# Performance work log

Hardware: AMD Instinct MI355X
Metric: run time of the kernel (lower is better)

Reference implementation:

```python
import jax, jax.numpy as jnp
import numpy as np

N_NODES = 20000
N_INPUT = 64
K_MAX = 12
BITS = 64
N_OUT = 10
BATCH = 64
T = 128


def setup_inputs() -> dict:
    key = jax.random.key(0)
    ks = jax.random.split(key, 8)
    x = jax.random.randint(ks[0], (BATCH, T, BITS), 0, 2, dtype=jnp.int32)
    w_in = jax.random.randint(ks[1], (BITS, N_INPUT), 0, 2, dtype=jnp.int32)
    adj_list = jax.random.randint(ks[2], (N_NODES, K_MAX), 0, N_NODES, dtype=jnp.int32)
    adj_mask = jax.random.randint(ks[3], (N_NODES, K_MAX), 0, 2, dtype=jnp.int32)
    lut = jax.random.randint(ks[4], (N_NODES, 2 ** K_MAX), 0, 2, dtype=jnp.int32)
    init_states = jax.random.randint(ks[5], (1, N_NODES), 0, 2, dtype=jnp.int32)
    W_out = jax.random.normal(ks[6], (N_OUT, N_NODES - N_INPUT), dtype=jnp.float32) * 0.02
    b_out = jnp.zeros((N_OUT,), dtype=jnp.float32)
    return {"x": x, "w_in": w_in, "adj_list": adj_list, "adj_mask": adj_mask,
            "lut": lut, "init_states": init_states, "W_out": W_out, "b_out": b_out}


def reference(x, w_in, adj_list, adj_mask, lut, init_states, W_out, b_out):
    B, T_, bits = x.shape
    N, k = adj_list.shape
    I = w_in.shape[1]
    # powers_of_2, big-endian order as in make_minimal_powers_of_two (flip)
    powers = (2 ** jnp.arange(k - 1, -1, -1)).astype(jnp.int32)  # [k]
    no_neigh = ~(adj_mask.astype(bool).any(axis=1))              # [N] nodes w/o neighbours keep state
    node_ids = jnp.arange(N)
    states0 = jnp.broadcast_to(init_states, (B, N)).astype(jnp.int32)

    def step(states, x_t):
        # inject input: bipartite mapping of input bits onto first I nodes (OR-combine)
        u = ((x_t @ w_in) > 0).astype(jnp.int32)                 # [B, I]
        states = states.at[:, :I].set(u)
        # gather incoming neighbour states per node (irregular gather)
        neigh = jnp.take(states, adj_list, axis=1)               # [B, N, k]
        neigh = neigh * adj_mask[None, :, :]
        # bit-pack into LUT index
        idx = (neigh * powers[None, None, :]).sum(axis=-1)       # [B, N], < 2^k
        new = lut[node_ids[None, :], idx]                        # [B, N] LUT lookup
        new = jnp.where(no_neigh[None, :], states, new)
        return new, None

    states, _ = jax.lax.scan(step, states0, jnp.swapaxes(x, 0, 1))
    # readout on reservoir (non-input) nodes at final timestep
    feats = states[:, I:].astype(jnp.float32)                    # [B, N-I]
    out = jax.nn.sigmoid(feats @ W_out.T + b_out)                # [B, n_outputs]
    return out
```

## Files before the change

### kernel.cpp

```cpp
#include <hip/hip_runtime.h>
#include <cstdint>
#include <cstddef>


#define N_NODES   20000
#define N_INPUT   64
#define K_MAX     12
#define T_STEPS   128
#define N_BATCH   64
#define N_OUT     10
#define N_FEAT    (N_NODES - N_INPUT)
#define DUMMY_NODE 20000
#define ST_WORDS  20004

#define NBLK 512
#define NTHR 512
#define NPB  39
#define NPB_PAD 40
#define BAR_CNT 64
#define GO_CNT  8
#define BAR_STRIDE 32

typedef unsigned long long u64;

__global__ __launch_bounds__(256) void pack_x_kernel(const int* __restrict__ x,
                                                     u64* __restrict__ xp) {
  const int t = blockIdx.x;
  const int wave = threadIdx.x >> 6, lane = threadIdx.x & 63;
  for (int b = wave; b < N_BATCH; b += 4) {
    int v = x[((size_t)b * T_STEPS + t) * 64 + lane];
    u64 bal = __ballot(v != 0);
    if (lane == 0) xp[(size_t)t * N_BATCH + b] = bal;
  }
}

__global__ __launch_bounds__(256) void init_kernel(const int* __restrict__ inis,
                                                   const int* __restrict__ w_in,
                                                   const u64* __restrict__ xp,
                                                   u64* __restrict__ buf0,
                                                   u64* __restrict__ buf1,
                                                   u64* __restrict__ wcol,
                                                   unsigned* __restrict__ bar) {
  if (blockIdx.x < 79) {
    int n = blockIdx.x * 256 + threadIdx.x;
    if (n >= N_INPUT && n < ST_WORDS) {
      u64 w = (n < N_NODES && inis[n] != 0) ? ~0ull : 0ull;
      buf0[n] = w;
      buf1[n] = w;
    }
  } else {
    const int wave = threadIdx.x >> 6, lane = threadIdx.x & 63;
    u64 xw = xp[lane];
    for (int i = wave; i < 64; i += 4) {
      int wv = w_in[(size_t)lane * 64 + i];
      u64 wc = __ballot(wv != 0);
      if (lane == 0) wcol[i] = wc;
      u64 ub = __ballot((xw & wc) != 0);
      if (lane == 0) buf0[i] = ub;
    }
    if (threadIdx.x < BAR_CNT + GO_CNT)
      bar[threadIdx.x * BAR_STRIDE] = 0u;
  }
}

__global__ __launch_bounds__(64) void u_pre_kernel(const u64* __restrict__ xp,
                                                   const u64* __restrict__ wcol,
                                                   u64* __restrict__ u_all) {
  const int t = blockIdx.x, lane = threadIdx.x;
  u64 xw = xp[(size_t)t * N_BATCH + lane];
  for (int i = 0; i < 64; i++) {
    u64 ub = __ballot((xw & wcol[i]) != 0);
    if (lane == 0) u_all[(size_t)t * 64 + i] = ub;
  }
}

__device__ __forceinline__ u64 bit_transpose64(u64 w, int lane) {
  const u64 LO0 = 0x00000000FFFFFFFFull, LO1 = 0x0000FFFF0000FFFFull,
            LO2 = 0x00FF00FF00FF00FFull, LO3 = 0x0F0F0F0F0F0F0F0Full,
            LO4 = 0x3333333333333333ull, LO5 = 0x5555555555555555ull;
#define XP_STAGE(d, LO)                                                  \
  {                                                                      \
    u64 p = (u64)__shfl_xor((long long)w, (d), 64);                      \
    if (lane & (d)) w = ((p >> (d)) & (LO)) | (w & ~(LO));               \
    else            w = (w & (LO)) | ((p << (d)) & ~(LO));               \
  }
  XP_STAGE(32, LO0) XP_STAGE(16, LO1) XP_STAGE(8, LO2)
  XP_STAGE(4,  LO3) XP_STAGE(2,  LO4) XP_STAGE(1, LO5)
#undef XP_STAGE
  return w;
}

__global__ __launch_bounds__(NTHR, 4) void reservoir_kernel(
    const int* __restrict__ lut, const int* __restrict__ adj,
    const int* __restrict__ mask, const u64* __restrict__ u_all,
    u64* __restrict__ buf0, u64* __restrict__ buf1,
    unsigned* __restrict__ bar) {
  __shared__ u64 lut_lds[NPB_PAD * 64];
  __shared__ int adj_lds[NPB_PAD * K_MAX];
  __shared__ unsigned char hn_lds[NPB_PAD];

  const int bi = blockIdx.x;
  const int tid = threadIdx.x;
  const int wave = tid >> 6, lane = tid & 63;
  const int base = N_INPUT + bi * NPB;
  const int nloc = min(NPB, N_NODES - base);

  if (tid < NPB_PAD) {
    int i = tid, h = 0;
    if (i < nloc) {
      for (int j = 0; j < K_MAX; j++) {
        int m = mask[(size_t)(base + i) * K_MAX + j];
        int a = adj[(size_t)(base + i) * K_MAX + j];
        adj_lds[i * K_MAX + (K_MAX - 1 - j)] = m ? a : DUMMY_NODE;
        h |= m;
      }
    } else {
      for (int j = 0; j < K_MAX; j++) adj_lds[i * K_MAX + j] = DUMMY_NODE;
    }
    hn_lds[i] = (unsigned char)(h ? 1 : 0);
  }

  const int nwords = nloc * 64;
  const int* lp = lut + (size_t)base * 4096;
  for (int w0 = wave * 8; w0 < nwords; w0 += 64) {
    int v[8];
#pragma unroll
    for (int q = 0; q < 8; q++) {
      int widx = w0 + q;
      v[q] = (widx < nwords) ? lp[(size_t)widx * 64 + lane] : 0;
    }
#pragma unroll
    for (int q = 0; q < 8; q++) {
      int widx = w0 + q;
      u64 bal = __ballot(v[q] != 0);
      if (lane == 0 && widx < nwords) lut_lds[widx] = bal;
    }
  }
  __syncthreads();

  const int l0 = wave * 5;
  const int cnt = min(5, nloc - l0);

  int my_a = DUMMY_NODE;
  if (lane < 60) my_a = adj_lds[l0 * K_MAX + lane];
  unsigned hmask = 0;
#pragma unroll
  for (int i = 0; i < 5; i++) hmask |= (unsigned)hn_lds[l0 + i] << i;

  for (int t = 0; t < T_STEPS; t++) {
    u64* cur = (t & 1) ? buf1 : buf0;
    u64* nxt = (t & 1) ? buf0 : buf1;

    u64 w = __hip_atomic_load(&cur[my_a], __ATOMIC_RELAXED,
                              __HIP_MEMORY_SCOPE_AGENT);
    w = bit_transpose64(w, lane);

#pragma unroll
    for (int i = 0; i < 5; i++) {
      if (i < cnt) {
        unsigned idx = (unsigned)(w >> (12 * i)) & 0xFFFu;
        u64 g = lut_lds[(l0 + i) * 64 + (idx >> 6)];
        u64 res = __ballot((g >> (idx & 63)) & 1ull);
        if (lane == 0 && ((hmask >> i) & 1u))
          __hip_atomic_store(&nxt[base + l0 + i], res,
                             __ATOMIC_RELAXED, __HIP_MEMORY_SCOPE_AGENT);
      }
    }

    if (bi == NBLK - 1 && wave == 7 && t + 1 < T_STEPS) {
      u64 uw = u_all[(size_t)(t + 1) * 64 + lane];
      __hip_atomic_store(&nxt[lane], uw, __ATOMIC_RELAXED, __HIP_MEMORY_SCOPE_AGENT);
    }

    if (t != T_STEPS - 1) {
      __syncthreads();
      __builtin_amdgcn_fence(__ATOMIC_RELEASE, "workgroup");
      if (tid == 0)
        __hip_atomic_fetch_add(&bar[(bi & (BAR_CNT - 1)) * BAR_STRIDE], 1u,
                               __ATOMIC_RELAXED, __HIP_MEMORY_SCOPE_AGENT);
      if (bi == 0 && wave == 0) {
        const unsigned tgt = (unsigned)(t + 1) * (NBLK / BAR_CNT);
        for (;;) {
          unsigned c = __hip_atomic_load(&bar[lane * BAR_STRIDE],
                                         __ATOMIC_RELAXED, __HIP_MEMORY_SCOPE_AGENT);
          if (__all(c >= tgt)) break;
        }
        if (lane < GO_CNT)
          __hip_atomic_store(&bar[(BAR_CNT + lane) * BAR_STRIDE], (unsigned)(t + 1),
                             __ATOMIC_RELAXED, __HIP_MEMORY_SCOPE_AGENT);
      } else if (wave == 0) {
        unsigned* gp = &bar[(BAR_CNT + (bi & (GO_CNT - 1))) * BAR_STRIDE];
        while (__hip_atomic_load(gp, __ATOMIC_RELAXED, __HIP_MEMORY_SCOPE_AGENT)
               < (unsigned)(t + 1)) {  }
      }
      __builtin_amdgcn_fence(__ATOMIC_ACQUIRE, "workgroup");
      __syncthreads();
    }
  }
}

__global__ __launch_bounds__(256) void readout_kernel(const u64* __restrict__ st,
                                                      const float* __restrict__ Wout,
                                                      const float* __restrict__ bout,
                                                      float* __restrict__ out) {
  const int b = blockIdx.x / N_OUT;
  const int o = blockIdx.x % N_OUT;
  float acc = 0.f;
  for (int n = threadIdx.x; n < N_FEAT; n += 256) {
    u64 s = st[N_INPUT + n];
    float w = Wout[(size_t)o * N_FEAT + n];
    acc += ((s >> b) & 1ull) ? w : 0.f;
  }
  for (int off = 32; off > 0; off >>= 1) acc += __shfl_down(acc, off);
  __shared__ float red[4];
  const int wave = threadIdx.x >> 6, lane = threadIdx.x & 63;
  if (lane == 0) red[wave] = acc;
  __syncthreads();
  if (threadIdx.x == 0) {
    float tot = red[0] + red[1] + red[2] + red[3] + bout[o];
    out[(size_t)b * N_OUT + o] = 1.f / (1.f + __expf(-tot));
  }
}

extern "C" void kernel_launch(void* const* d_in, const int* in_sizes, int n_in,
                              void* d_out, int out_size, void* d_ws, size_t ws_size,
                              hipStream_t stream) {
  const int* x    = (const int*)d_in[0];
  const int* w_in = (const int*)d_in[1];
  const int* adj  = (const int*)d_in[2];
  const int* mask = (const int*)d_in[3];
  const int* lut  = (const int*)d_in[4];
  const int* inis = (const int*)d_in[5];
  const float* Wout = (const float*)d_in[6];
  const float* bout = (const float*)d_in[7];
  float* out = (float*)d_out;

  char* ws = (char*)d_ws;
  size_t off = 0;
  auto alloc = [&](size_t bytes) -> void* {
    void* p = ws + off;
    off += (bytes + 255) & ~(size_t)255;
    return p;
  };
  u64* buf0 = (u64*)alloc((size_t)ST_WORDS * 8);
  u64* buf1 = (u64*)alloc((size_t)ST_WORDS * 8);
  u64* xp   = (u64*)alloc((size_t)T_STEPS * N_BATCH * 8);
  u64* wcol = (u64*)alloc(64 * 8);
  u64* u_all = (u64*)alloc((size_t)T_STEPS * 64 * 8);
  unsigned* bar = (unsigned*)alloc((size_t)(BAR_CNT + GO_CNT) * BAR_STRIDE * 4);
  (void)ws_size; (void)in_sizes; (void)n_in; (void)out_size;

  hipLaunchKernelGGL(pack_x_kernel, dim3(T_STEPS), dim3(256), 0, stream, x, xp);
  hipLaunchKernelGGL(init_kernel, dim3(80), dim3(256), 0, stream,
                     inis, w_in, xp, buf0, buf1, wcol, bar);
  hipLaunchKernelGGL(u_pre_kernel, dim3(T_STEPS), dim3(64), 0, stream,
                     xp, wcol, u_all);

  hipLaunchKernelGGL(reservoir_kernel, dim3(NBLK), dim3(NTHR), 0, stream,
                     lut, adj, mask, u_all, buf0, buf1, bar);

  hipLaunchKernelGGL(readout_kernel, dim3(N_BATCH * N_OUT), dim3(256), 0, stream,
                     buf0, Wout, bout, out);
}
```

Before: 963.8 us.

## Fuse input prep kernels and split readout into chunked partial reduction

Merges the x-packing, init and per-step input projection kernels into one prep kernel. Each block computes its own packed x and w_in columns in shared memory, which removes two launches and their global round-trips. The readout is restructured so each thread handles one batch bit over a node chunk, with a second tiny kernel summing the partials and applying the sigmoid. This cuts redundant reads of the state and weights, since the old version had each of 640 blocks scan all nodes. The cost is an extra small launch plus redundant w_in packing in every prep block.

```diff
diff --git a/kernel.cpp b/kernel.cpp
--- a/kernel.cpp
+++ b/kernel.cpp
@@ -21,56 +21,52 @@
 #define GO_CNT  8
 #define BAR_STRIDE 32
 
+#define RO_CHUNK 32
+#define RO_NPC   623
+
 typedef unsigned long long u64;
 
-__global__ __launch_bounds__(256) void pack_x_kernel(const int* __restrict__ x,
-                                                     u64* __restrict__ xp) {
-  const int t = blockIdx.x;
-  const int wave = threadIdx.x >> 6, lane = threadIdx.x & 63;
-  for (int b = wave; b < N_BATCH; b += 4) {
-    int v = x[((size_t)b * T_STEPS + t) * 64 + lane];
-    u64 bal = __ballot(v != 0);
-    if (lane == 0) xp[(size_t)t * N_BATCH + b] = bal;
-  }
-}
-
-__global__ __launch_bounds__(256) void init_kernel(const int* __restrict__ inis,
+__global__ __launch_bounds__(256) void prep_kernel(const int* __restrict__ x,
                                                    const int* __restrict__ w_in,
-                                                   const u64* __restrict__ xp,
+                                                   const int* __restrict__ inis,
                                                    u64* __restrict__ buf0,
                                                    u64* __restrict__ buf1,
-                                                   u64* __restrict__ wcol,
+                                                   u64* __restrict__ u_all,
                                                    unsigned* __restrict__ bar) {
-  if (blockIdx.x < 79) {
-    int n = blockIdx.x * 256 + threadIdx.x;
+  const int wave = threadIdx.x >> 6, lane = threadIdx.x & 63;
+  if (blockIdx.x < T_STEPS) {
+    const int t = blockIdx.x;
+    __shared__ u64 xp_lds[N_BATCH];
+    __shared__ u64 wcol_lds[64];
+    for (int b = wave; b < N_BATCH; b += 4) {
+      int v = x[((size_t)b * T_STEPS + t) * 64 + lane];
+      u64 bal = __ballot(v != 0);
+      if (lane == 0) xp_lds[b] = bal;
+    }
+    for (int i = wave; i < 64; i += 4) {
+      int wv = w_in[(size_t)lane * 64 + i];
+      u64 wc = __ballot(wv != 0);
+      if (lane == 0) wcol_lds[i] = wc;
+    }
+    __syncthreads();
+    u64 xw = xp_lds[lane];
+    for (int i = wave; i < 64; i += 4) {
+      u64 ub = __ballot((xw & wcol_lds[i]) != 0);
+      if (lane == 0) {
+        if (t == 0) buf0[i] = ub;
+        else        u_all[(size_t)t * 64 + i] = ub;
+      }
+    }
+  } else if (blockIdx.x < T_STEPS + 79) {
+    int n = (blockIdx.x - T_STEPS) * 256 + threadIdx.x;
     if (n >= N_INPUT && n < ST_WORDS) {
       u64 w = (n < N_NODES && inis[n] != 0) ? ~0ull : 0ull;
       buf0[n] = w;
       buf1[n] = w;
     }
   } else {
-    const int wave = threadIdx.x >> 6, lane = threadIdx.x & 63;
-    u64 xw = xp[lane];
-    for (int i = wave; i < 64; i += 4) {
-      int wv = w_in[(size_t)lane * 64 + i];
-      u64 wc = __ballot(wv != 0);
-      if (lane == 0) wcol[i] = wc;
-      u64 ub = __ballot((xw & wc) != 0);
-      if (lane == 0) buf0[i] = ub;
-    }
     if (threadIdx.x < BAR_CNT + GO_CNT)
       bar[threadIdx.x * BAR_STRIDE] = 0u;
-  }
-}
-
-__global__ __launch_bounds__(64) void u_pre_kernel(const u64* __restrict__ xp,
-                                                   const u64* __restrict__ wcol,
-                                                   u64* __restrict__ u_all) {
-  const int t = blockIdx.x, lane = threadIdx.x;
-  u64 xw = xp[(size_t)t * N_BATCH + lane];
-  for (int i = 0; i < 64; i++) {
-    u64 ub = __ballot((xw & wcol[i]) != 0);
-    if (lane == 0) u_all[(size_t)t * 64 + i] = ub;
   }
 }
 
@@ -199,27 +195,36 @@
   }
 }
 
-__global__ __launch_bounds__(256) void readout_kernel(const u64* __restrict__ st,
-                                                      const float* __restrict__ Wout,
-                                                      const float* __restrict__ bout,
-                                                      float* __restrict__ out) {
-  const int b = blockIdx.x / N_OUT;
+__global__ __launch_bounds__(256) void readout_part(const u64* __restrict__ st,
+                                                    const float* __restrict__ Wout,
+                                                    float* __restrict__ partial) {
+  const int c = blockIdx.x / N_OUT;
   const int o = blockIdx.x % N_OUT;
+  const int b = threadIdx.x & 63, k = threadIdx.x >> 6;
+  const int n0 = c * RO_NPC, n1 = n0 + RO_NPC;
   float acc = 0.f;
-  for (int n = threadIdx.x; n < N_FEAT; n += 256) {
+  for (int n = n0 + k; n < n1; n += 4) {
     u64 s = st[N_INPUT + n];
     float w = Wout[(size_t)o * N_FEAT + n];
     acc += ((s >> b) & 1ull) ? w : 0.f;
   }
-  for (int off = 32; off > 0; off >>= 1) acc += __shfl_down(acc, off);
-  __shared__ float red[4];
-  const int wave = threadIdx.x >> 6, lane = threadIdx.x & 63;
-  if (lane == 0) red[wave] = acc;
+  __shared__ float red[4][64];
+  red[k][b] = acc;
   __syncthreads();
-  if (threadIdx.x == 0) {
-    float tot = red[0] + red[1] + red[2] + red[3] + bout[o];
-    out[(size_t)b * N_OUT + o] = 1.f / (1.f + __expf(-tot));
-  }
+  if (threadIdx.x < 64) {
+    float tot = red[0][b] + red[1][b] + red[2][b] + red[3][b];
+    partial[((size_t)c * N_OUT + o) * 64 + b] = tot;
+  }
+}
+
+__global__ __launch_bounds__(640) void readout_final(const float* __restrict__ partial,
+                                                     const float* __restrict__ bout,
+                                                     float* __restrict__ out) {
+  const int b = threadIdx.x & 63, o = threadIdx.x >> 6;
+  float tot = bout[o];
+  for (int c = 0; c < RO_CHUNK; c++)
+    tot += partial[((size_t)c * N_OUT + o) * 64 + b];
+  out[(size_t)b * N_OUT + o] = 1.f / (1.f + __expf(-tot));
 }
 
 extern "C" void kernel_launch(void* const* d_in, const int* in_sizes, int n_in,
@@ -244,21 +249,19 @@
   };
   u64* buf0 = (u64*)alloc((size_t)ST_WORDS * 8);
   u64* buf1 = (u64*)alloc((size_t)ST_WORDS * 8);
-  u64* xp   = (u64*)alloc((size_t)T_STEPS * N_BATCH * 8);
-  u64* wcol = (u64*)alloc(64 * 8);
   u64* u_all = (u64*)alloc((size_t)T_STEPS * 64 * 8);
   unsigned* bar = (unsigned*)alloc((size_t)(BAR_CNT + GO_CNT) * BAR_STRIDE * 4);
+  float* partial = (float*)alloc((size_t)RO_CHUNK * N_OUT * 64 * 4);
   (void)ws_size; (void)in_sizes; (void)n_in; (void)out_size;
 
-  hipLaunchKernelGGL(pack_x_kernel, dim3(T_STEPS), dim3(256), 0, stream, x, xp);
-  hipLaunchKernelGGL(init_kernel, dim3(80), dim3(256), 0, stream,
-                     inis, w_in, xp, buf0, buf1, wcol, bar);
-  hipLaunchKernelGGL(u_pre_kernel, dim3(T_STEPS), dim3(64), 0, stream,
-                     xp, wcol, u_all);
+  hipLaunchKernelGGL(prep_kernel, dim3(T_STEPS + 79 + 1), dim3(256), 0, stream,
+                     x, w_in, inis, buf0, buf1, u_all, bar);
 
   hipLaunchKernelGGL(reservoir_kernel, dim3(NBLK), dim3(NTHR), 0, stream,
                      lut, adj, mask, u_all, buf0, buf1, bar);
 
-  hipLaunchKernelGGL(readout_kernel, dim3(N_BATCH * N_OUT), dim3(256), 0, stream,
-                     buf0, Wout, bout, out);
-}
+  hipLaunchKernelGGL(readout_part, dim3(RO_CHUNK * N_OUT), dim3(256), 0, stream,
+                     buf0, Wout, partial);
+  hipLaunchKernelGGL(readout_final, dim3(1), dim3(640), 0, stream,
+                     partial, bout, out);
+}
```

Result: no change. 967.5 us (+0.4%).
